# Kernel tuning notes

Measured on AMD Instinct MI355X. Metric: run time of the kernel, lower is better.

Reference implementation:

```python
import jax, jax.numpy as jnp
import numpy as np

EPS = 1e-5

def _layernorm(x, g, b):
    m = jnp.mean(x, axis=-1, keepdims=True)
    v = jnp.mean(jnp.square(x - m), axis=-1, keepdims=True)
    return (x - m) * jax.lax.rsqrt(v + EPS) * g + b

def setup_inputs() -> dict:
    key = jax.random.key(0)
    ks = jax.random.split(key, 8)
    B, T, C, H, D = 4096, 16, 512, 8, 64
    s = 0.02
    return {
        "x": jax.random.normal(ks[0], (B, T, C), jnp.float32),
        "ln1_g": jnp.ones((C,), jnp.float32),
        "ln1_b": jnp.zeros((C,), jnp.float32),
        "wq": jax.random.normal(ks[1], (H, C, D), jnp.float32) * s,
        "wk": jax.random.normal(ks[2], (H, C, D), jnp.float32) * s,
        "wv": jax.random.normal(ks[3], (H, C, D), jnp.float32) * s,
        "w_proj": jax.random.normal(ks[4], (H * D, C), jnp.float32) * s,
        "b_proj": jnp.zeros((C,), jnp.float32),
        "ln2_g": jnp.ones((C,), jnp.float32),
        "ln2_b": jnp.zeros((C,), jnp.float32),
        "w1": jax.random.normal(ks[5], (C, 4 * C), jnp.float32) * s,
        "b1": jnp.zeros((4 * C,), jnp.float32),
        "w2": jax.random.normal(ks[6], (4 * C, C), jnp.float32) * s,
        "b2": jnp.zeros((C,), jnp.float32),
    }

def reference(x, ln1_g, ln1_b, wq, wk, wv, w_proj, b_proj, ln2_g, ln2_b, w1, b1, w2, b2):
    B, T, C = x.shape
    H, _, D = wq.shape
    h = _layernorm(x, ln1_g, ln1_b)
    # fused per-head projections (original looped over 8 Head modules)
    q = jnp.einsum('btc,hcd->bhtd', h, wq)
    k = jnp.einsum('btc,hcd->bhtd', h, wk)
    v = jnp.einsum('btc,hcd->bhtd', h, wv)
    logits = jnp.einsum('bhtd,bhsd->bhts', q, k) * (D ** -0.5)
    causal = jnp.tril(jnp.ones((T, T), bool))
    logits = jnp.where(causal, logits, -jnp.inf)
    att = jax.nn.softmax(logits, axis=-1)  # dropout is identity at eval
    o = jnp.einsum('bhts,bhsd->bhtd', att, v)
    o = o.transpose(0, 2, 1, 3).reshape(B, T, H * D)  # concat heads in order
    y = o @ w_proj + b_proj + x  # residual 1
    h2 = _layernorm(y, ln2_g, ln2_b)
    f = jax.nn.relu(h2 @ w1 + b1) @ w2 + b2
    return f + y  # residual 2
```

## Files before the change

### kernel.cpp

```cpp
#include <hip/hip_runtime.h>
#include <hip/hip_bf16.h>

typedef __attribute__((ext_vector_type(8))) short s16x8;
typedef __attribute__((ext_vector_type(4))) short s16x4;
typedef __attribute__((ext_vector_type(4))) float f32x4;

#define GAS __attribute__((address_space(1)))
#define LAS __attribute__((address_space(3)))

#define WAITV(N) asm volatile("s_waitcnt vmcnt(" #N ")" ::: "memory")
#define WAITL() asm volatile("s_waitcnt lgkmcnt(0)" ::: "memory")
#define BAR() __builtin_amdgcn_s_barrier()

__device__ __forceinline__ float b2f(unsigned short u) {
  union { unsigned int i; float f; } x; x.i = ((unsigned int)u) << 16; return x.f;
}
__device__ __forceinline__ unsigned short f2b(float f) {
  union { float f; unsigned int i; } x; x.f = f;
  unsigned int r = x.i + 0x7fffu + ((x.i >> 16) & 1u);
  return (unsigned short)(r >> 16);
}

__device__ __forceinline__ void gl16(const unsigned short* g, unsigned short* l) {
  __builtin_amdgcn_global_load_lds((const GAS unsigned int*)g,
                                   (LAS unsigned int*)l, 16, 0, 0);
}

__global__ __launch_bounds__(256) void pack_qkv_k(const float* __restrict__ wq,
                                                  const float* __restrict__ wk,
                                                  const float* __restrict__ wv,
                                                  unsigned short* __restrict__ dst) {
  int idx = blockIdx.x * 256 + threadIdx.x;
  int n = idx >> 9, c = idx & 511;
  int sel = n >> 9;
  int hn = n & 511;
  const float* src = sel == 0 ? wq : (sel == 1 ? wk : wv);
  float v = src[((hn >> 6) << 15) + (c << 6) + (hn & 63)];
  dst[idx] = f2b(v);
}

__global__ __launch_bounds__(256) void pack_T_k(const float* __restrict__ src,
                                                unsigned short* __restrict__ dst,
                                                int K, int N) {
  int idx = blockIdx.x * 256 + threadIdx.x;
  int n = idx / K, k = idx % K;
  dst[idx] = f2b(src[(long long)k * N + n]);
}

__global__ __launch_bounds__(256) void ln_k(const float* __restrict__ in,
                                            const float* __restrict__ g,
                                            const float* __restrict__ bb,
                                            unsigned short* __restrict__ out) {
  int row = blockIdx.x * 4 + (threadIdx.x >> 6);
  int lane = threadIdx.x & 63;
  const float* p = in + (size_t)row * 512 + lane * 8;
  f32x4 a = *(const f32x4*)p;
  f32x4 b = *(const f32x4*)(p + 4);
  float vals[8] = {a.x, a.y, a.z, a.w, b.x, b.y, b.z, b.w};
  float s = 0.f, q = 0.f;
#pragma unroll
  for (int i = 0; i < 8; i++) { s += vals[i]; q += vals[i] * vals[i]; }
#pragma unroll
  for (int off = 1; off < 64; off <<= 1) {
    s += __shfl_xor(s, off);
    q += __shfl_xor(q, off);
  }
  float mean = s * (1.0f / 512.0f);
  float rstd = rsqrtf(q * (1.0f / 512.0f) - mean * mean + 1e-5f);
  const float* gp = g + lane * 8;
  const float* bp = bb + lane * 8;
  s16x8 o;
#pragma unroll
  for (int i = 0; i < 8; i++) o[i] = (short)f2b((vals[i] - mean) * rstd * gp[i] + bp[i]);
  *(s16x8*)(out + (size_t)row * 512 + lane * 8) = o;
}

__global__ __launch_bounds__(256) void ln_b_k(const unsigned short* __restrict__ in,
                                              const float* __restrict__ g,
                                              const float* __restrict__ bb,
                                              unsigned short* __restrict__ out) {
  int row = blockIdx.x * 4 + (threadIdx.x >> 6);
  int lane = threadIdx.x & 63;
  s16x8 v8 = *(const s16x8*)(in + (size_t)row * 512 + lane * 8);
  float vals[8];
#pragma unroll
  for (int i = 0; i < 8; i++) vals[i] = b2f((unsigned short)v8[i]);
  float s = 0.f, q = 0.f;
#pragma unroll
  for (int i = 0; i < 8; i++) { s += vals[i]; q += vals[i] * vals[i]; }
#pragma unroll
  for (int off = 1; off < 64; off <<= 1) {
    s += __shfl_xor(s, off);
    q += __shfl_xor(q, off);
  }
  float mean = s * (1.0f / 512.0f);
  float rstd = rsqrtf(q * (1.0f / 512.0f) - mean * mean + 1e-5f);
  const float* gp = g + lane * 8;
  const float* bp = bb + lane * 8;
  s16x8 o;
#pragma unroll
  for (int i = 0; i < 8; i++) o[i] = (short)f2b((vals[i] - mean) * rstd * gp[i] + bp[i]);
  *(s16x8*)(out + (size_t)row * 512 + lane * 8) = o;
}

__global__ __launch_bounds__(256) void attn_k(const unsigned short* __restrict__ qkv,
                                              unsigned short* __restrict__ o) {
  int w = (blockIdx.x << 2) + (threadIdx.x >> 6);
  int lane = threadIdx.x & 63;
  int b = w >> 3, h = w & 7;
  int t = lane >> 2, p = lane & 3;

  size_t rowq = (size_t)(b * 16 + t) * 1536 + h * 64 + p * 16;
  float q[16];
  {
    s16x8 q0 = *(const s16x8*)(qkv + rowq);
    s16x8 q1 = *(const s16x8*)(qkv + rowq + 8);
#pragma unroll
    for (int i = 0; i < 8; i++) {
      q[i] = b2f((unsigned short)q0[i]) * 0.125f;
      q[8 + i] = b2f((unsigned short)q1[i]) * 0.125f;
    }
  }
  float lg[16];
  size_t kbase = (size_t)(b * 16) * 1536 + 512 + h * 64 + p * 16;
#pragma unroll
  for (int s = 0; s < 16; s++) {
    const unsigned short* kp = qkv + kbase + (size_t)s * 1536;
    s16x8 k0 = *(const s16x8*)kp;
    s16x8 k1 = *(const s16x8*)(kp + 8);
    float d = 0.f;
#pragma unroll
    for (int i = 0; i < 8; i++)
      d += q[i] * b2f((unsigned short)k0[i]) + q[8 + i] * b2f((unsigned short)k1[i]);
    d += __shfl_xor(d, 1);
    d += __shfl_xor(d, 2);
    lg[s] = d;
  }
  float mx = -1e30f;
#pragma unroll
  for (int s = 0; s < 16; s++)
    if (s <= t) mx = fmaxf(mx, lg[s]);
  float den = 0.f;
#pragma unroll
  for (int s = 0; s < 16; s++) {
    float e = (s <= t) ? __expf(lg[s] - mx) : 0.f;
    lg[s] = e;
    den += e;
  }
  float inv = 1.f / den;
  float acc[16] = {};
  size_t vbase = kbase + 512;
#pragma unroll
  for (int s = 0; s < 16; s++) {
    const unsigned short* vp = qkv + vbase + (size_t)s * 1536;
    s16x8 v0 = *(const s16x8*)vp;
    s16x8 v1 = *(const s16x8*)(vp + 8);
    float a = lg[s] * inv;
#pragma unroll
    for (int i = 0; i < 8; i++) {
      acc[i] += a * b2f((unsigned short)v0[i]);
      acc[8 + i] += a * b2f((unsigned short)v1[i]);
    }
  }
  size_t orow = (size_t)(b * 16 + t) * 512 + h * 64 + p * 16;
  s16x8 r0, r1;
#pragma unroll
  for (int i = 0; i < 8; i++) {
    r0[i] = (short)f2b(acc[i]);
    r1[i] = (short)f2b(acc[8 + i]);
  }
  *(s16x8*)(o + orow) = r0;
  *(s16x8*)(o + orow + 8) = r1;
}

enum { EPI_BF16 = 0, EPI_RESF32 = 1, EPI_RELU_BF16 = 2, EPI_YB = 3, EPI_OUTB = 4 };

template <int EPI>
__global__ __launch_bounds__(512, 2) void gemm_bt(
    const unsigned short* __restrict__ A,
    const unsigned short* __restrict__ Bt,
    int K, int N, int nT,
    const float* __restrict__ bias, const void* __restrict__ res,
    float* __restrict__ outF, unsigned short* __restrict__ outB) {
  __shared__ __align__(16) unsigned char SM[131072];

  int tid = threadIdx.x;
  int lid = ((int)blockIdx.x & 7) * ((int)gridDim.x >> 3) + ((int)blockIdx.x >> 3);
  int mBase = (lid / nT) * 256;
  int nBase = (lid % nT) * 256;

  int lane = tid & 63;
  int wid = tid >> 6;
  int wm = wid >> 2;
  int wn = wid & 3;
  int l15 = lane & 15;
  int s4 = lane >> 4;
  int lr4 = s4 * 4;
  int fc = ((s4 ^ ((l15 >> 1) & 3)) << 3);

  int srow = tid >> 2;
  int scol = (((tid & 3) ^ ((tid >> 3) & 3)) << 3);
  const unsigned short* pa = A + (size_t)(mBase + srow) * K + scol;
  const unsigned short* pb = Bt + (size_t)(nBase + srow) * K + scol;
  size_t k128 = (size_t)128 * K;

  f32x4 acc[8][4] = {};

  auto stage = [&](int buf, int kt) {
    unsigned short* dA = (unsigned short*)(SM + buf * 32768) + wid * 512;
    unsigned short* dB = (unsigned short*)(SM + buf * 32768 + 16384) + wid * 512;
    gl16(pa + kt, dA);
    gl16(pa + kt + k128, dA + 4096);
    gl16(pb + kt, dB);
    gl16(pb + kt + k128, dB + 4096);
  };

  auto computeT = [&](int buf) {
    const unsigned short* hA = (const unsigned short*)(SM + buf * 32768) + wm * 4096;
    const unsigned short* hB = (const unsigned short*)(SM + buf * 32768 + 16384) + wn * 2048;
    s16x8 bfr[4], afr[4];
#pragma unroll
    for (int n = 0; n < 4; ++n)
      bfr[n] = *(const s16x8*)&hB[(n * 16 + l15) * 32 + fc];
#pragma unroll
    for (int m = 0; m < 4; ++m)
      afr[m] = *(const s16x8*)&hA[(m * 16 + l15) * 32 + fc];
    __builtin_amdgcn_s_setprio(1);
#pragma unroll
    for (int m = 0; m < 4; ++m)
#pragma unroll
      for (int n = 0; n < 4; ++n)
        acc[m][n] = __builtin_amdgcn_mfma_f32_16x16x32_bf16(afr[m], bfr[n], acc[m][n], 0, 0, 0);
    __builtin_amdgcn_s_setprio(0);
#pragma unroll
    for (int m = 0; m < 4; ++m)
      afr[m] = *(const s16x8*)&hA[((m + 4) * 16 + l15) * 32 + fc];
    __builtin_amdgcn_s_setprio(1);
#pragma unroll
    for (int m = 0; m < 4; ++m)
#pragma unroll
      for (int n = 0; n < 4; ++n)
        acc[m + 4][n] = __builtin_amdgcn_mfma_f32_16x16x32_bf16(afr[m], bfr[n], acc[m + 4][n], 0, 0, 0);
    __builtin_amdgcn_s_setprio(0);
  };

  int NT = K >> 5;
  stage(0, 0);
  stage(1, 32);
  stage(2, 64);
  for (int t = 0; t < NT - 3; ++t) {
    stage((t + 3) & 3, (t + 3) << 5);
    WAITV(12);
    BAR();
    computeT(t & 3);
    BAR();
  }
  WAITV(8);  BAR(); computeT((NT - 3) & 3); BAR();
  WAITV(4);  BAR(); computeT((NT - 2) & 3); BAR();
  WAITV(0);  BAR(); computeT((NT - 1) & 3);
  BAR();

  if (EPI == EPI_RESF32 || EPI == EPI_OUTB) {
#pragma unroll
    for (int n = 0; n < 4; n++) {
      int gc2 = nBase + wn * 64 + n * 16 + l15;
      float bv = bias[gc2];
#pragma unroll
      for (int m = 0; m < 8; m++) {
#pragma unroll
        for (int j = 0; j < 4; j++) {
          int gr = mBase + wm * 128 + m * 16 + lr4 + j;
          size_t off = (size_t)gr * N + gc2;
          float v = acc[m][n][j] + bv;
          if (EPI == EPI_RESF32)
            outF[off] = v + ((const float*)res)[off];
          else
            outF[off] = v + b2f(((const unsigned short*)res)[off]);
        }
      }
    }
  } else {
    float* ep = (float*)SM + wid * 1088;
    int colc = nBase + wn * 64 + (lane & 15) * 4;
    f32x4 bias4 = {0.f, 0.f, 0.f, 0.f};
    if (EPI != EPI_BF16) bias4 = *(const f32x4*)&bias[colc];
#pragma unroll
    for (int m = 0; m < 8; m++) {
#pragma unroll
      for (int n = 0; n < 4; n++)
#pragma unroll
        for (int j = 0; j < 4; j++)
          ep[(lr4 + j) * 68 + n * 16 + l15] = acc[m][n][j];
      WAITL();
#pragma unroll
      for (int rd = 0; rd < 4; rd++) {
        int r = (lane >> 4) + 4 * rd;
        f32x4 v = *(const f32x4*)&ep[r * 68 + (lane & 15) * 4];
        v.x += bias4.x; v.y += bias4.y; v.z += bias4.z; v.w += bias4.w;
        int gr = mBase + wm * 128 + m * 16 + r;
        size_t off = (size_t)gr * N + colc;
        if (EPI == EPI_YB) {
          f32x4 rv = *(const f32x4*)&((const float*)res)[off];
          v.x += rv.x; v.y += rv.y; v.z += rv.z; v.w += rv.w;
        } else if (EPI == EPI_RELU_BF16) {
          v.x = fmaxf(v.x, 0.f); v.y = fmaxf(v.y, 0.f);
          v.z = fmaxf(v.z, 0.f); v.w = fmaxf(v.w, 0.f);
        }
        s16x4 o;
        o[0] = (short)f2b(v.x); o[1] = (short)f2b(v.y);
        o[2] = (short)f2b(v.z); o[3] = (short)f2b(v.w);
        *(s16x4*)(outB + off) = o;
      }
      WAITL();
    }
  }
}

extern "C" void kernel_launch(void* const* d_in, const int* in_sizes, int n_in,
                              void* d_out, int out_size, void* d_ws, size_t ws_size,
                              hipStream_t stream) {
  const float* x      = (const float*)d_in[0];
  const float* ln1_g  = (const float*)d_in[1];
  const float* ln1_b  = (const float*)d_in[2];
  const float* wq     = (const float*)d_in[3];
  const float* wk     = (const float*)d_in[4];
  const float* wv     = (const float*)d_in[5];
  const float* w_proj = (const float*)d_in[6];
  const float* b_proj = (const float*)d_in[7];
  const float* ln2_g  = (const float*)d_in[8];
  const float* ln2_b  = (const float*)d_in[9];
  const float* w1     = (const float*)d_in[10];
  const float* b1     = (const float*)d_in[11];
  const float* w2     = (const float*)d_in[12];
  const float* b2     = (const float*)d_in[13];
  float* out = (float*)d_out;

  char* ws = (char*)d_ws;
  unsigned short* qkvT  = (unsigned short*)(ws + 0);
  unsigned short* projT = (unsigned short*)(ws + 1572864);
  unsigned short* w1T   = (unsigned short*)(ws + 2097152);
  unsigned short* w2T   = (unsigned short*)(ws + 4194304);
  unsigned short* hbuf  = (unsigned short*)(ws + 6291456);
  unsigned short* qkv   = (unsigned short*)(ws + 73400320);
  unsigned short* obuf  = (unsigned short*)(ws + 341835776);
  unsigned short* ybuf  = (unsigned short*)(ws + 408944640);
  bool yb16 = ws_size >= 476053504ull;

  pack_qkv_k<<<3072, 256, 0, stream>>>(wq, wk, wv, qkvT);
  pack_T_k<<<1024, 256, 0, stream>>>(w_proj, projT, 512, 512);
  pack_T_k<<<4096, 256, 0, stream>>>(w1, w1T, 512, 2048);
  pack_T_k<<<4096, 256, 0, stream>>>(w2, w2T, 2048, 512);

  ln_k<<<16384, 256, 0, stream>>>(x, ln1_g, ln1_b, hbuf);

  gemm_bt<EPI_BF16><<<1536, 512, 0, stream>>>(hbuf, qkvT, 512, 1536, 6,
                                              nullptr, nullptr, nullptr, qkv);
  attn_k<<<8192, 256, 0, stream>>>(qkv, obuf);

  unsigned short* ff = qkv;
  if (yb16) {
    gemm_bt<EPI_YB><<<512, 512, 0, stream>>>(obuf, projT, 512, 512, 2,
                                             b_proj, x, nullptr, ybuf);
    ln_b_k<<<16384, 256, 0, stream>>>(ybuf, ln2_g, ln2_b, hbuf);
    gemm_bt<EPI_RELU_BF16><<<2048, 512, 0, stream>>>(hbuf, w1T, 512, 2048, 8,
                                                     b1, nullptr, nullptr, ff);
    gemm_bt<EPI_OUTB><<<512, 512, 0, stream>>>(ff, w2T, 2048, 512, 2,
                                               b2, ybuf, out, nullptr);
  } else {
    gemm_bt<EPI_RESF32><<<512, 512, 0, stream>>>(obuf, projT, 512, 512, 2,
                                                 b_proj, x, out, nullptr);
    ln_k<<<16384, 256, 0, stream>>>(out, ln2_g, ln2_b, hbuf);
    gemm_bt<EPI_RELU_BF16><<<2048, 512, 0, stream>>>(hbuf, w1T, 512, 2048, 8,
                                                     b1, nullptr, nullptr, ff);
    gemm_bt<EPI_RESF32><<<512, 512, 0, stream>>>(ff, w2T, 2048, 512, 2,
                                                 b2, out, out, nullptr);
  }
}
```

Before: 788.6 us.

## Restructure GEMM pipeline to triple buffering with interleaved half-tile loads

Shared memory for the bf16 GEMM drops from four 32KB stages to three, and the three buffers now rotate. Each tile's global-to-LDS loads are split into A and B halves, issued between the two MFMA half-blocks with extra barriers and sched_barrier fences so memory traffic interleaves with compute. The aim is to cut the LDS footprint and smooth the issue schedule. In exchange the prefetch distance is shorter and each iteration has more barriers.

```diff
diff --git a/kernel.cpp b/kernel.cpp
--- a/kernel.cpp
+++ b/kernel.cpp
@@ -11,6 +11,7 @@
 #define WAITV(N) asm volatile("s_waitcnt vmcnt(" #N ")" ::: "memory")
 #define WAITL() asm volatile("s_waitcnt lgkmcnt(0)" ::: "memory")
 #define BAR() __builtin_amdgcn_s_barrier()
+#define SCHED0() __builtin_amdgcn_sched_barrier(0)
 
 __device__ __forceinline__ float b2f(unsigned short u) {
   union { unsigned int i; float f; } x; x.i = ((unsigned int)u) << 16; return x.f;
@@ -182,7 +183,7 @@
     int K, int N, int nT,
     const float* __restrict__ bias, const void* __restrict__ res,
     float* __restrict__ outF, unsigned short* __restrict__ outB) {
-  __shared__ __align__(16) unsigned char SM[131072];
+  __shared__ __align__(16) unsigned char SM[98304];
 
   int tid = threadIdx.x;
   int lid = ((int)blockIdx.x & 7) * ((int)gridDim.x >> 3) + ((int)blockIdx.x >> 3);
@@ -206,7 +207,7 @@
 
   f32x4 acc[8][4] = {};
 
-  auto stage = [&](int buf, int kt) {
+  auto stageFull = [&](int buf, int kt) {
     unsigned short* dA = (unsigned short*)(SM + buf * 32768) + wid * 512;
     unsigned short* dB = (unsigned short*)(SM + buf * 32768 + 16384) + wid * 512;
     gl16(pa + kt, dA);
@@ -215,7 +216,7 @@
     gl16(pb + kt + k128, dB + 4096);
   };
 
-  auto computeT = [&](int buf) {
+  auto tileBody = [&](int buf, int stg, int sbuf, int kt2) {
     const unsigned short* hA = (const unsigned short*)(SM + buf * 32768) + wm * 4096;
     const unsigned short* hB = (const unsigned short*)(SM + buf * 32768 + 16384) + wn * 2048;
     s16x8 bfr[4], afr[4];
@@ -225,6 +226,13 @@
 #pragma unroll
     for (int m = 0; m < 4; ++m)
       afr[m] = *(const s16x8*)&hA[(m * 16 + l15) * 32 + fc];
+    if (stg) {
+      unsigned short* dA = (unsigned short*)(SM + sbuf * 32768) + wid * 512;
+      gl16(pa + kt2, dA);
+      gl16(pa + kt2 + k128, dA + 4096);
+    }
+    BAR();
+    WAITL(); SCHED0();
     __builtin_amdgcn_s_setprio(1);
 #pragma unroll
     for (int m = 0; m < 4; ++m)
@@ -232,9 +240,17 @@
       for (int n = 0; n < 4; ++n)
         acc[m][n] = __builtin_amdgcn_mfma_f32_16x16x32_bf16(afr[m], bfr[n], acc[m][n], 0, 0, 0);
     __builtin_amdgcn_s_setprio(0);
+    BAR();
 #pragma unroll
     for (int m = 0; m < 4; ++m)
       afr[m] = *(const s16x8*)&hA[((m + 4) * 16 + l15) * 32 + fc];
+    if (stg) {
+      unsigned short* dB = (unsigned short*)(SM + sbuf * 32768 + 16384) + wid * 512;
+      gl16(pb + kt2, dB);
+      gl16(pb + kt2 + k128, dB + 4096);
+    }
+    BAR();
+    WAITL(); SCHED0();
     __builtin_amdgcn_s_setprio(1);
 #pragma unroll
     for (int m = 0; m < 4; ++m)
@@ -242,22 +258,26 @@
       for (int n = 0; n < 4; ++n)
         acc[m + 4][n] = __builtin_amdgcn_mfma_f32_16x16x32_bf16(afr[m], bfr[n], acc[m + 4][n], 0, 0, 0);
     __builtin_amdgcn_s_setprio(0);
+    BAR();
   };
 
   int NT = K >> 5;
-  stage(0, 0);
-  stage(1, 32);
-  stage(2, 64);
-  for (int t = 0; t < NT - 3; ++t) {
-    stage((t + 3) & 3, (t + 3) << 5);
-    WAITV(12);
-    BAR();
-    computeT(t & 3);
-    BAR();
-  }
-  WAITV(8);  BAR(); computeT((NT - 3) & 3); BAR();
-  WAITV(4);  BAR(); computeT((NT - 2) & 3); BAR();
-  WAITV(0);  BAR(); computeT((NT - 1) & 3);
+  stageFull(0, 0);
+  stageFull(1, 32);
+  WAITV(4);
+  BAR();
+  int t = 0;
+  int b0 = 0, b1 = 1, b2 = 2;
+  for (; t < NT - 2; ++t) {
+    tileBody(b0, 1, b2, (t + 2) << 5);
+    WAITV(4);
+    BAR();
+    int tmp = b0; b0 = b1; b1 = b2; b2 = tmp;
+  }
+  tileBody(b0, 0, 0, 0);
+  WAITV(0);
+  BAR();
+  tileBody(b1, 0, 0, 0);
   BAR();
 
   if (EPI == EPI_RESF32 || EPI == EPI_OUTB) {
```

New measurement: 752.9 us. 4.5% less time.

## Restructure GEMM staging into split A/B half-tile prefetch and pack x to bf16

Applied to the files above, without the earlier changes.

The GEMM main loop now issues the A and B half-tiles as separate loads into a 4-slot ring. B for step t+2 is prefetched before the compute barrier and A for step t+3 mid-iteration, with an extra barrier between the two MFMA halves. This aims to spread global-to-LDS traffic through the iteration instead of issuing it in bursts. The launch bounds no longer request two blocks per CU, the LDS swizzle index changes, and x is converted to bf16 once and reused for LN1 and the first residual, which cuts f32 reads but rounds the residual to bf16.

```diff
diff --git a/kernel.cpp b/kernel.cpp
--- a/kernel.cpp
+++ b/kernel.cpp
@@ -24,6 +24,18 @@
 __device__ __forceinline__ void gl16(const unsigned short* g, unsigned short* l) {
   __builtin_amdgcn_global_load_lds((const GAS unsigned int*)g,
                                    (LAS unsigned int*)l, 16, 0, 0);
+}
+
+__global__ __launch_bounds__(256) void pack_x_k(const float* __restrict__ x,
+                                                unsigned short* __restrict__ xb) {
+  size_t i = ((size_t)blockIdx.x * 256 + threadIdx.x) * 8;
+  f32x4 a = *(const f32x4*)(x + i);
+  f32x4 b = *(const f32x4*)(x + i + 4);
+  float vals[8] = {a.x, a.y, a.z, a.w, b.x, b.y, b.z, b.w};
+  s16x8 o;
+#pragma unroll
+  for (int k = 0; k < 8; k++) o[k] = (short)f2b(vals[k]);
+  *(s16x8*)(xb + i) = o;
 }
 
 __global__ __launch_bounds__(256) void pack_qkv_k(const float* __restrict__ wq,
@@ -173,10 +185,10 @@
   *(s16x8*)(o + orow + 8) = r1;
 }
 
-enum { EPI_BF16 = 0, EPI_RESF32 = 1, EPI_RELU_BF16 = 2, EPI_YB = 3, EPI_OUTB = 4 };
+enum { EPI_BF16 = 0, EPI_RESF32 = 1, EPI_RELU = 2, EPI_YBB = 3, EPI_OUTB = 4 };
 
 template <int EPI>
-__global__ __launch_bounds__(512, 2) void gemm_bt(
+__global__ __launch_bounds__(512) void gemm_bt(
     const unsigned short* __restrict__ A,
     const unsigned short* __restrict__ Bt,
     int K, int N, int nT,
@@ -199,65 +211,77 @@
   int fc = ((s4 ^ ((l15 >> 1) & 3)) << 3);
 
   int srow = tid >> 2;
-  int scol = (((tid & 3) ^ ((tid >> 3) & 3)) << 3);
+  int scol = (((tid & 3) ^ ((srow >> 1) & 3)) << 3);
   const unsigned short* pa = A + (size_t)(mBase + srow) * K + scol;
   const unsigned short* pb = Bt + (size_t)(nBase + srow) * K + scol;
   size_t k128 = (size_t)128 * K;
+  unsigned short* dstB = (unsigned short*)SM + wid * 512;
 
   f32x4 acc[8][4] = {};
 
-  auto stage = [&](int buf, int kt) {
-    unsigned short* dA = (unsigned short*)(SM + buf * 32768) + wid * 512;
-    unsigned short* dB = (unsigned short*)(SM + buf * 32768 + 16384) + wid * 512;
-    gl16(pa + kt, dA);
-    gl16(pa + kt + k128, dA + 4096);
-    gl16(pb + kt, dB);
-    gl16(pb + kt + k128, dB + 4096);
+  auto stgA = [&](int slot, int a, int t) {
+    gl16(pa + (size_t)a * k128 + t * 32, dstB + slot * 4096);
   };
-
-  auto computeT = [&](int buf) {
-    const unsigned short* hA = (const unsigned short*)(SM + buf * 32768) + wm * 4096;
-    const unsigned short* hB = (const unsigned short*)(SM + buf * 32768 + 16384) + wn * 2048;
-    s16x8 bfr[4], afr[4];
+  auto stgB = [&](int slot, int b, int t) {
+    gl16(pb + (size_t)b * k128 + t * 32, dstB + slot * 4096);
+  };
+
+  int NT = K >> 5;
+  stgA(0, 0, 0);  stgA(1, 1, 0);
+  stgB(2, 0, 0);  stgB(3, 1, 0);
+  stgA(4, 0, 1);  stgA(5, 1, 1);
+  stgB(6, 0, 1);  stgB(7, 1, 1);
+  stgA(8, 0, 2);  stgA(9, 1, 2);
+
+  for (int t = 0; t < NT; ++t) {
+    int sb = (t & 3) << 2;
+    const unsigned short* hA = (const unsigned short*)SM + (size_t)(sb + wm) * 4096;
+    const unsigned short* hB = (const unsigned short*)SM + (size_t)(sb + 2 + (wn >> 1)) * 4096;
+    int br = (wn & 1) * 64;
+    s16x8 af[4], bf[4];
+
+    if (t + 2 < NT) {
+      int s2 = ((t + 2) & 3) << 2;
+      stgB(s2 + 2, 0, t + 2);
+      stgB(s2 + 3, 1, t + 2);
+      WAITV(8);
+    } else if (t == NT - 2) {
+      WAITV(4);
+    } else {
+      WAITV(0);
+    }
+    BAR();
 #pragma unroll
     for (int n = 0; n < 4; ++n)
-      bfr[n] = *(const s16x8*)&hB[(n * 16 + l15) * 32 + fc];
+      bf[n] = *(const s16x8*)&hB[(br + n * 16 + l15) * 32 + fc];
 #pragma unroll
     for (int m = 0; m < 4; ++m)
-      afr[m] = *(const s16x8*)&hA[(m * 16 + l15) * 32 + fc];
+      af[m] = *(const s16x8*)&hA[(m * 16 + l15) * 32 + fc];
     __builtin_amdgcn_s_setprio(1);
 #pragma unroll
     for (int m = 0; m < 4; ++m)
 #pragma unroll
       for (int n = 0; n < 4; ++n)
-        acc[m][n] = __builtin_amdgcn_mfma_f32_16x16x32_bf16(afr[m], bfr[n], acc[m][n], 0, 0, 0);
+        acc[m][n] = __builtin_amdgcn_mfma_f32_16x16x32_bf16(af[m], bf[n], acc[m][n], 0, 0, 0);
     __builtin_amdgcn_s_setprio(0);
+
 #pragma unroll
     for (int m = 0; m < 4; ++m)
-      afr[m] = *(const s16x8*)&hA[((m + 4) * 16 + l15) * 32 + fc];
+      af[m] = *(const s16x8*)&hA[((m + 4) * 16 + l15) * 32 + fc];
+    if (t + 3 < NT) {
+      int s3 = ((t + 3) & 3) << 2;
+      stgA(s3 + 0, 0, t + 3);
+      stgA(s3 + 1, 1, t + 3);
+    }
+    BAR();
     __builtin_amdgcn_s_setprio(1);
 #pragma unroll
     for (int m = 0; m < 4; ++m)
 #pragma unroll
       for (int n = 0; n < 4; ++n)
-        acc[m + 4][n] = __builtin_amdgcn_mfma_f32_16x16x32_bf16(afr[m], bfr[n], acc[m + 4][n], 0, 0, 0);
+        acc[m + 4][n] = __builtin_amdgcn_mfma_f32_16x16x32_bf16(af[m], bf[n], acc[m + 4][n], 0, 0, 0);
     __builtin_amdgcn_s_setprio(0);
-  };
-
-  int NT = K >> 5;
-  stage(0, 0);
-  stage(1, 32);
-  stage(2, 64);
-  for (int t = 0; t < NT - 3; ++t) {
-    stage((t + 3) & 3, (t + 3) << 5);
-    WAITV(12);
-    BAR();
-    computeT(t & 3);
-    BAR();
-  }
-  WAITV(8);  BAR(); computeT((NT - 3) & 3); BAR();
-  WAITV(4);  BAR(); computeT((NT - 2) & 3); BAR();
-  WAITV(0);  BAR(); computeT((NT - 1) & 3);
+  }
   BAR();
 
   if (EPI == EPI_RESF32 || EPI == EPI_OUTB) {
@@ -281,7 +305,7 @@
     }
   } else {
     float* ep = (float*)SM + wid * 1088;
-    int colc = nBase + wn * 64 + (lane & 15) * 4;
+    int colc = nBase + wn * 64 + l15 * 4;
     f32x4 bias4 = {0.f, 0.f, 0.f, 0.f};
     if (EPI != EPI_BF16) bias4 = *(const f32x4*)&bias[colc];
 #pragma unroll
@@ -294,15 +318,16 @@
       WAITL();
 #pragma unroll
       for (int rd = 0; rd < 4; rd++) {
-        int r = (lane >> 4) + 4 * rd;
-        f32x4 v = *(const f32x4*)&ep[r * 68 + (lane & 15) * 4];
+        int r = s4 + 4 * rd;
+        f32x4 v = *(const f32x4*)&ep[r * 68 + l15 * 4];
         v.x += bias4.x; v.y += bias4.y; v.z += bias4.z; v.w += bias4.w;
         int gr = mBase + wm * 128 + m * 16 + r;
         size_t off = (size_t)gr * N + colc;
-        if (EPI == EPI_YB) {
-          f32x4 rv = *(const f32x4*)&((const float*)res)[off];
-          v.x += rv.x; v.y += rv.y; v.z += rv.z; v.w += rv.w;
-        } else if (EPI == EPI_RELU_BF16) {
+        if (EPI == EPI_YBB) {
+          s16x4 rb = *(const s16x4*)((const unsigned short*)res + off);
+          v.x += b2f((unsigned short)rb[0]); v.y += b2f((unsigned short)rb[1]);
+          v.z += b2f((unsigned short)rb[2]); v.w += b2f((unsigned short)rb[3]);
+        } else if (EPI == EPI_RELU) {
           v.x = fmaxf(v.x, 0.f); v.y = fmaxf(v.y, 0.f);
           v.z = fmaxf(v.z, 0.f); v.w = fmaxf(v.w, 0.f);
         }
@@ -342,6 +367,7 @@
   unsigned short* w2T   = (unsigned short*)(ws + 4194304);
   unsigned short* hbuf  = (unsigned short*)(ws + 6291456);
   unsigned short* qkv   = (unsigned short*)(ws + 73400320);
+  unsigned short* xb    = (unsigned short*)(ws + 274726912);
   unsigned short* obuf  = (unsigned short*)(ws + 341835776);
   unsigned short* ybuf  = (unsigned short*)(ws + 408944640);
   bool yb16 = ws_size >= 476053504ull;
@@ -351,27 +377,30 @@
   pack_T_k<<<4096, 256, 0, stream>>>(w1, w1T, 512, 2048);
   pack_T_k<<<4096, 256, 0, stream>>>(w2, w2T, 2048, 512);
 
-  ln_k<<<16384, 256, 0, stream>>>(x, ln1_g, ln1_b, hbuf);
-
-  gemm_bt<EPI_BF16><<<1536, 512, 0, stream>>>(hbuf, qkvT, 512, 1536, 6,
-                                              nullptr, nullptr, nullptr, qkv);
-  attn_k<<<8192, 256, 0, stream>>>(qkv, obuf);
-
   unsigned short* ff = qkv;
   if (yb16) {
-    gemm_bt<EPI_YB><<<512, 512, 0, stream>>>(obuf, projT, 512, 512, 2,
-                                             b_proj, x, nullptr, ybuf);
+    pack_x_k<<<16384, 256, 0, stream>>>(x, xb);
+    ln_b_k<<<16384, 256, 0, stream>>>(xb, ln1_g, ln1_b, hbuf);
+    gemm_bt<EPI_BF16><<<1536, 512, 0, stream>>>(hbuf, qkvT, 512, 1536, 6,
+                                                nullptr, nullptr, nullptr, qkv);
+    attn_k<<<8192, 256, 0, stream>>>(qkv, obuf);
+    gemm_bt<EPI_YBB><<<512, 512, 0, stream>>>(obuf, projT, 512, 512, 2,
+                                              b_proj, xb, nullptr, ybuf);
     ln_b_k<<<16384, 256, 0, stream>>>(ybuf, ln2_g, ln2_b, hbuf);
-    gemm_bt<EPI_RELU_BF16><<<2048, 512, 0, stream>>>(hbuf, w1T, 512, 2048, 8,
-                                                     b1, nullptr, nullptr, ff);
+    gemm_bt<EPI_RELU><<<2048, 512, 0, stream>>>(hbuf, w1T, 512, 2048, 8,
+                                                b1, nullptr, nullptr, ff);
     gemm_bt<EPI_OUTB><<<512, 512, 0, stream>>>(ff, w2T, 2048, 512, 2,
                                                b2, ybuf, out, nullptr);
   } else {
+    ln_k<<<16384, 256, 0, stream>>>(x, ln1_g, ln1_b, hbuf);
+    gemm_bt<EPI_BF16><<<1536, 512, 0, stream>>>(hbuf, qkvT, 512, 1536, 6,
+                                                nullptr, nullptr, nullptr, qkv);
+    attn_k<<<8192, 256, 0, stream>>>(qkv, obuf);
     gemm_bt<EPI_RESF32><<<512, 512, 0, stream>>>(obuf, projT, 512, 512, 2,
                                                  b_proj, x, out, nullptr);
     ln_k<<<16384, 256, 0, stream>>>(out, ln2_g, ln2_b, hbuf);
-    gemm_bt<EPI_RELU_BF16><<<2048, 512, 0, stream>>>(hbuf, w1T, 512, 2048, 8,
-                                                     b1, nullptr, nullptr, ff);
+    gemm_bt<EPI_RELU><<<2048, 512, 0, stream>>>(hbuf, w1T, 512, 2048, 8,
+                                                b1, nullptr, nullptr, ff);
     gemm_bt<EPI_RESF32><<<512, 512, 0, stream>>>(ff, w2T, 2048, 512, 2,
                                                  b2, out, out, nullptr);
   }
```

New measurement: 760.0 us, median of 2. 1.04x faster.
